# Optimization experiments

Hardware: AMD Instinct MI355X
Metric: run time of the kernel (lower is better)

## Reference

```python
import jax, jax.numpy as jnp
import numpy as np


def _compute_deltas(ts, m):
    """Affine time-decay recurrence: delta_0 = 0; for t>=1:
    delta_t = gap_t + (1 - m_{t-1}) * delta_{t-1}, with gap broadcast over features.
    ts: [b, s] timestamps, m: [b, s, f] float 0/1 mask. Returns [b, s, f]."""
    b, s, f = m.shape
    gaps = ts[:, 1:] - ts[:, :-1]          # [b, s-1]
    a = 1.0 - m[:, :-1, :]                 # [b, s-1, f] decay coefficient

    def step(d, inp):
        g_t, a_t = inp                      # g_t: [b], a_t: [b, f]
        d = g_t[:, None] + a_t * d
        return d, d

    gT = jnp.swapaxes(gaps, 0, 1)          # [s-1, b]
    aT = jnp.swapaxes(a, 0, 1)             # [s-1, b, f]
    _, ds = jax.lax.scan(step, jnp.zeros((b, f), ts.dtype), (gT, aT))
    ds = jnp.swapaxes(ds, 0, 1)            # [b, s-1, f]
    return jnp.concatenate([jnp.zeros((b, 1, f), ts.dtype), ds], axis=1)


def setup_inputs() -> dict:
    key = jax.random.key(0)
    k1, k2, k3 = jax.random.split(key, 3)
    b, s, f = 32, 2048, 768
    # monotonically increasing timestamps (cumsum of positive gaps)
    gaps = jax.random.uniform(k1, (b, s), minval=1.0, maxval=60.0, dtype=jnp.float32)
    timestamps = jnp.cumsum(gaps, axis=1)
    encoded_data = jax.random.normal(k2, (b, s, f), dtype=jnp.float32)
    masks = jax.random.randint(k3, (b, s, f), 0, 2, dtype=jnp.int32)
    return {"timestamps": timestamps, "encoded_data": encoded_data, "masks": masks}


def reference(timestamps, encoded_data, masks):
    """JAX translation of _prepare_brits_data. Returns stacked
    [forward_deltas, backward_deltas, backward_X] of shape [3, b, s, f].
    (forward X / masks are pass-through inputs; backward mask is flip(masks).)"""
    m = masks.astype(timestamps.dtype)
    forward_deltas = _compute_deltas(timestamps, m)
    ts_b = jnp.flip(timestamps, axis=1)
    m_b = jnp.flip(m, axis=1)
    backward_deltas = jnp.abs(_compute_deltas(ts_b, m_b))
    x_b = jnp.flip(encoded_data, axis=1)
    return jnp.stack([forward_deltas, backward_deltas, x_b], axis=0)
```

## Files before the change

### kernel.cpp

```cpp
#include <hip/hip_runtime.h>
#include <stdint.h>

static constexpr int B = 32, S = 2048, F = 768;
static constexpr int CS = 128;
static constexpr int NCH = S / CS;
static constexpr int FT = F / 4;

__device__ __forceinline__ uint32_t getw(const uint4& v, int w) {
    switch (w) { case 0: return v.x; case 1: return v.y; case 2: return v.z; default: return v.w; }
}

__global__ __launch_bounds__(FT) void passA(const int* __restrict__ masks, uint4* __restrict__ bm) {
    const int blk = blockIdx.x;
    const int b = blk / NCH, c = blk % NCH;
    const int j = threadIdx.x;
    const int4* mp = reinterpret_cast<const int4*>(masks + ((size_t)b * S + (size_t)c * CS) * F) + j;
    uint32_t r[4][4];
    #pragma unroll
    for (int w = 0; w < 4; ++w) {
        uint32_t a0 = 0, a1 = 0, a2 = 0, a3 = 0;
        #pragma unroll 8
        for (int k2 = 0; k2 < 32; ++k2) {
            int4 mv = mp[(size_t)(w * 32 + k2) * (F / 4)];
            uint32_t bit = 1u << k2;
            if (mv.x) a0 |= bit;
            if (mv.y) a1 |= bit;
            if (mv.z) a2 |= bit;
            if (mv.w) a3 |= bit;
        }
        r[w][0] = a0; r[w][1] = a1; r[w][2] = a2; r[w][3] = a3;
    }
    uint4* op = bm + (size_t)blk * F + 4 * j;
    #pragma unroll
    for (int q = 0; q < 4; ++q)
        op[q] = make_uint4(r[0][q], r[1][q], r[2][q], r[3][q]);
}

__global__ void passB(const float* __restrict__ ts, const uint4* __restrict__ bm,
                      float* __restrict__ fwdc, float* __restrict__ bwdc) {
    int idx = blockIdx.x * blockDim.x + threadIdx.x;
    if (idx >= B * F) return;
    int b = idx / F, f = idx - b * F;
    const float* tsb = ts + (size_t)b * S;
    float carry = tsb[0];
    for (int c = 0; c < NCH; ++c) {
        fwdc[((size_t)b * NCH + c) * F + f] = carry;
        uint4 v = bm[((size_t)b * NCH + c) * F + f];
        int base = c * CS;
        if (v.w)      carry = tsb[base + 96 + (31 - __clz((int)v.w))];
        else if (v.z) carry = tsb[base + 64 + (31 - __clz((int)v.z))];
        else if (v.y) carry = tsb[base + 32 + (31 - __clz((int)v.y))];
        else if (v.x) carry = tsb[base +      (31 - __clz((int)v.x))];
    }
    carry = tsb[S - 1];
    for (int c = NCH - 1; c >= 0; --c) {
        bwdc[((size_t)b * NCH + c) * F + f] = carry;
        uint4 v = bm[((size_t)b * NCH + c) * F + f];
        int base = c * CS;
        if (v.x)      carry = tsb[base +      (__ffs((int)v.x) - 1)];
        else if (v.y) carry = tsb[base + 32 + (__ffs((int)v.y) - 1)];
        else if (v.z) carry = tsb[base + 64 + (__ffs((int)v.z) - 1)];
        else if (v.w) carry = tsb[base + 96 + (__ffs((int)v.w) - 1)];
    }
}

__global__ __launch_bounds__(FT) void passC(const float* __restrict__ ts, const uint4* __restrict__ bm,
                                            const float* __restrict__ fwdc, const float* __restrict__ bwdc,
                                            float* __restrict__ out0, float* __restrict__ out1) {
    const int blk = blockIdx.x;
    const int b = blk / NCH, c = blk % NCH;
    const int j = threadIdx.x;
    __shared__ float tss[CS];
    for (int k = threadIdx.x; k < CS; k += FT) tss[k] = ts[(size_t)b * S + (size_t)c * CS + k];
    __syncthreads();

    const uint4* bp = bm + (size_t)blk * F + 4 * j;
    uint4 bv0 = bp[0], bv1 = bp[1], bv2 = bp[2], bv3 = bp[3];
    float4 pv = *reinterpret_cast<const float4*>(fwdc + (size_t)blk * F + 4 * j);
    float4 nv = *reinterpret_cast<const float4*>(bwdc + (size_t)blk * F + 4 * j);
    float p0 = pv.x, p1 = pv.y, p2 = pv.z, p3 = pv.w;
    float n0 = nv.x, n1 = nv.y, n2 = nv.z, n3 = nv.w;
    float4* o0 = reinterpret_cast<float4*>(out0 + ((size_t)b * S + (size_t)c * CS) * F) + j;
    float4* o1 = reinterpret_cast<float4*>(out1 + (size_t)b * S * F) + j;

    #pragma unroll
    for (int w = 0; w < 4; ++w) {
        uint32_t b0 = getw(bv0, w), b1 = getw(bv1, w), b2 = getw(bv2, w), b3 = getw(bv3, w);
        #pragma unroll 8
        for (int k2 = 0; k2 < 32; ++k2) {
            int k = w * 32 + k2;
            float t = tss[k];
            o0[(size_t)k * (F / 4)] = make_float4(t - p0, t - p1, t - p2, t - p3);
            p0 = ((b0 >> k2) & 1u) ? t : p0;
            p1 = ((b1 >> k2) & 1u) ? t : p1;
            p2 = ((b2 >> k2) & 1u) ? t : p2;
            p3 = ((b3 >> k2) & 1u) ? t : p3;
        }
    }
    #pragma unroll
    for (int w = 3; w >= 0; --w) {
        uint32_t b0 = getw(bv0, w), b1 = getw(bv1, w), b2 = getw(bv2, w), b3 = getw(bv3, w);
        #pragma unroll 8
        for (int k2 = 31; k2 >= 0; --k2) {
            int k = w * 32 + k2;
            float t = tss[k];
            int rr = (S - 1) - (c * CS + k);
            o1[(size_t)rr * (F / 4)] = make_float4(n0 - t, n1 - t, n2 - t, n3 - t);
            n0 = ((b0 >> k2) & 1u) ? t : n0;
            n1 = ((b1 >> k2) & 1u) ? t : n1;
            n2 = ((b2 >> k2) & 1u) ? t : n2;
            n3 = ((b3 >> k2) & 1u) ? t : n3;
        }
    }
}

__global__ __launch_bounds__(FT) void passD(const float4* __restrict__ x, float4* __restrict__ o2) {
    const int r0 = blockIdx.x * 4;
    const int j = threadIdx.x;
    #pragma unroll
    for (int i = 0; i < 4; ++i) {
        int r = r0 + i;
        int b = r >> 11, t = r & (S - 1);
        int sr = (b << 11) + (S - 1 - t);
        o2[(size_t)r * (F / 4) + j] = x[(size_t)sr * (F / 4) + j];
    }
}

__global__ void fallbackK(const float* __restrict__ ts, const int* __restrict__ masks,
                          float* __restrict__ out0, float* __restrict__ out1) {
    int idx = blockIdx.x * blockDim.x + threadIdx.x;
    if (idx >= B * F) return;
    int b = idx / F, f = idx - b * F;
    const float* tsb = ts + (size_t)b * S;
    const int* mb = masks + (size_t)b * S * F + f;
    float* o0 = out0 + (size_t)b * S * F + f;
    float* o1 = out1 + (size_t)b * S * F + f;
    float prev = tsb[0];
    for (int t = 0; t < S; ++t) {
        float tt = tsb[t];
        o0[(size_t)t * F] = tt - prev;
        if (mb[(size_t)t * F]) prev = tt;
    }
    float nxt = tsb[S - 1];
    for (int t = S - 1; t >= 0; --t) {
        float tt = tsb[t];
        o1[(size_t)(S - 1 - t) * F] = nxt - tt;
        if (mb[(size_t)t * F]) nxt = tt;
    }
}

extern "C" void kernel_launch(void* const* d_in, const int* in_sizes, int n_in,
                              void* d_out, int out_size, void* d_ws, size_t ws_size,
                              hipStream_t stream) {
    const float* ts    = (const float*)d_in[0];
    const float* x     = (const float*)d_in[1];
    const int*   masks = (const int*)d_in[2];
    float* out = (float*)d_out;
    const size_t N = (size_t)B * S * F;

    const size_t bm_bytes    = (size_t)B * NCH * F * sizeof(uint4);
    const size_t carry_elems = (size_t)B * NCH * F;
    const size_t needed      = bm_bytes + 2 * carry_elems * sizeof(float);

    if (ws_size >= needed) {
        uint4* bm   = (uint4*)d_ws;
        float* fwdc = (float*)((char*)d_ws + bm_bytes);
        float* bwdc = fwdc + carry_elems;
        passA<<<B * NCH, FT, 0, stream>>>(masks, bm);
        passB<<<(B * F + 255) / 256, 256, 0, stream>>>(ts, bm, fwdc, bwdc);
        passC<<<B * NCH, FT, 0, stream>>>(ts, bm, fwdc, bwdc, out, out + N);
    } else {
        fallbackK<<<(B * F + 255) / 256, 256, 0, stream>>>(ts, masks, out, out + N);
    }
    passD<<<(B * S) / 4, FT, 0, stream>>>((const float4*)x, (float4*)(out + 2 * N));
}
```

Measured before the change: 239.9 us.

## Fuse mask packing, carry scan, delta output and flip copy into one kernel

Replaces the four-kernel pipeline (bitmask pack, per-chunk carry scan, delta write, reversed copy) with one kernel. Each block handles a 64-step chunk and finds its incoming forward and backward carries by scanning the raw masks outward from the chunk until a set bit is found. The flipped encoded_data copy is done in the same kernel. This removes the workspace bitmask and carry round-trips and several launches, but the carry search costs depend on mask density and can degrade badly for sparse masks.

Result: no change. 238.2 us (-0.7%).

```diff
diff --git a/kernel.cpp b/kernel.cpp
--- a/kernel.cpp
+++ b/kernel.cpp
@@ -2,150 +2,129 @@
 #include <stdint.h>
 
 static constexpr int B = 32, S = 2048, F = 768;
-static constexpr int CS = 128;
-static constexpr int NCH = S / CS;
-static constexpr int FT = F / 4;
+static constexpr int SC = 64;
+static constexpr int NSC = S / SC;
+static constexpr int F4 = F / 4;
+static constexpr int FT = F4;
 
-__device__ __forceinline__ uint32_t getw(const uint4& v, int w) {
-    switch (w) { case 0: return v.x; case 1: return v.y; case 2: return v.z; default: return v.w; }
-}
+__global__ __launch_bounds__(FT) void fusedK(const float* __restrict__ ts,
+                                             const float4* __restrict__ x,
+                                             const int4* __restrict__ masks,
+                                             float* __restrict__ out) {
+    const int blk = blockIdx.x;
+    const int b  = blk >> 5;
+    const int sc = blk & (NSC - 1);
+    const int g0 = sc * SC;
+    const int j  = threadIdx.x;
+    const float* tsb = ts + (size_t)b * S;
+    const int4* mbase = masks + (size_t)b * S * F4 + j;
 
-__global__ __launch_bounds__(FT) void passA(const int* __restrict__ masks, uint4* __restrict__ bm) {
-    const int blk = blockIdx.x;
-    const int b = blk / NCH, c = blk % NCH;
-    const int j = threadIdx.x;
-    const int4* mp = reinterpret_cast<const int4*>(masks + ((size_t)b * S + (size_t)c * CS) * F) + j;
-    uint32_t r[4][4];
-    #pragma unroll
-    for (int w = 0; w < 4; ++w) {
-        uint32_t a0 = 0, a1 = 0, a2 = 0, a3 = 0;
-        #pragma unroll 8
-        for (int k2 = 0; k2 < 32; ++k2) {
-            int4 mv = mp[(size_t)(w * 32 + k2) * (F / 4)];
-            uint32_t bit = 1u << k2;
-            if (mv.x) a0 |= bit;
-            if (mv.y) a1 |= bit;
-            if (mv.z) a2 |= bit;
-            if (mv.w) a3 |= bit;
-        }
-        r[w][0] = a0; r[w][1] = a1; r[w][2] = a2; r[w][3] = a3;
-    }
-    uint4* op = bm + (size_t)blk * F + 4 * j;
-    #pragma unroll
-    for (int q = 0; q < 4; ++q)
-        op[q] = make_uint4(r[0][q], r[1][q], r[2][q], r[3][q]);
-}
-
-__global__ void passB(const float* __restrict__ ts, const uint4* __restrict__ bm,
-                      float* __restrict__ fwdc, float* __restrict__ bwdc) {
-    int idx = blockIdx.x * blockDim.x + threadIdx.x;
-    if (idx >= B * F) return;
-    int b = idx / F, f = idx - b * F;
-    const float* tsb = ts + (size_t)b * S;
-    float carry = tsb[0];
-    for (int c = 0; c < NCH; ++c) {
-        fwdc[((size_t)b * NCH + c) * F + f] = carry;
-        uint4 v = bm[((size_t)b * NCH + c) * F + f];
-        int base = c * CS;
-        if (v.w)      carry = tsb[base + 96 + (31 - __clz((int)v.w))];
-        else if (v.z) carry = tsb[base + 64 + (31 - __clz((int)v.z))];
-        else if (v.y) carry = tsb[base + 32 + (31 - __clz((int)v.y))];
-        else if (v.x) carry = tsb[base +      (31 - __clz((int)v.x))];
-    }
-    carry = tsb[S - 1];
-    for (int c = NCH - 1; c >= 0; --c) {
-        bwdc[((size_t)b * NCH + c) * F + f] = carry;
-        uint4 v = bm[((size_t)b * NCH + c) * F + f];
-        int base = c * CS;
-        if (v.x)      carry = tsb[base +      (__ffs((int)v.x) - 1)];
-        else if (v.y) carry = tsb[base + 32 + (__ffs((int)v.y) - 1)];
-        else if (v.z) carry = tsb[base + 64 + (__ffs((int)v.z) - 1)];
-        else if (v.w) carry = tsb[base + 96 + (__ffs((int)v.w) - 1)];
-    }
-}
-
-__global__ __launch_bounds__(FT) void passC(const float* __restrict__ ts, const uint4* __restrict__ bm,
-                                            const float* __restrict__ fwdc, const float* __restrict__ bwdc,
-                                            float* __restrict__ out0, float* __restrict__ out1) {
-    const int blk = blockIdx.x;
-    const int b = blk / NCH, c = blk % NCH;
-    const int j = threadIdx.x;
-    __shared__ float tss[CS];
-    for (int k = threadIdx.x; k < CS; k += FT) tss[k] = ts[(size_t)b * S + (size_t)c * CS + k];
+    __shared__ float tss[SC];
+    if (threadIdx.x < SC) tss[threadIdx.x] = tsb[g0 + threadIdx.x];
     __syncthreads();
 
-    const uint4* bp = bm + (size_t)blk * F + 4 * j;
-    uint4 bv0 = bp[0], bv1 = bp[1], bv2 = bp[2], bv3 = bp[3];
-    float4 pv = *reinterpret_cast<const float4*>(fwdc + (size_t)blk * F + 4 * j);
-    float4 nv = *reinterpret_cast<const float4*>(bwdc + (size_t)blk * F + 4 * j);
-    float p0 = pv.x, p1 = pv.y, p2 = pv.z, p3 = pv.w;
-    float n0 = nv.x, n1 = nv.y, n2 = nv.z, n3 = nv.w;
-    float4* o0 = reinterpret_cast<float4*>(out0 + ((size_t)b * S + (size_t)c * CS) * F) + j;
-    float4* o1 = reinterpret_cast<float4*>(out1 + (size_t)b * S * F) + j;
+    float t0v = tsb[0];
+    float p0 = t0v, p1 = t0v, p2 = t0v, p3 = t0v;
+    if (g0 > 0) {
+        unsigned um = 0xFu;
+        int r = g0 - 1;
+        while (um && r >= 0) {
+            int rl = (r - 7 > 0) ? r - 7 : 0;
+            int nn = r - rl + 1;
+            int4 mv[8];
+            #pragma unroll
+            for (int q = 0; q < 8; ++q) if (q < nn) mv[q] = mbase[(size_t)(r - q) * F4];
+            #pragma unroll
+            for (int q = 0; q < 8; ++q) if (q < nn) {
+                float t = tsb[r - q];
+                if ((um & 1u) && mv[q].x) { p0 = t; um &= ~1u; }
+                if ((um & 2u) && mv[q].y) { p1 = t; um &= ~2u; }
+                if ((um & 4u) && mv[q].z) { p2 = t; um &= ~4u; }
+                if ((um & 8u) && mv[q].w) { p3 = t; um &= ~8u; }
+            }
+            r = rl - 1;
+        }
+    }
+
+    float tev = tsb[S - 1];
+    float n0 = tev, n1 = tev, n2 = tev, n3 = tev;
+    if (g0 + SC < S) {
+        unsigned um = 0xFu;
+        int r = g0 + SC;
+        while (um && r < S) {
+            int rh = (r + 7 < S - 1) ? r + 7 : S - 1;
+            int nn = rh - r + 1;
+            int4 mv[8];
+            #pragma unroll
+            for (int q = 0; q < 8; ++q) if (q < nn) mv[q] = mbase[(size_t)(r + q) * F4];
+            #pragma unroll
+            for (int q = 0; q < 8; ++q) if (q < nn) {
+                float t = tsb[r + q];
+                if ((um & 1u) && mv[q].x) { n0 = t; um &= ~1u; }
+                if ((um & 2u) && mv[q].y) { n1 = t; um &= ~2u; }
+                if ((um & 4u) && mv[q].z) { n2 = t; um &= ~4u; }
+                if ((um & 8u) && mv[q].w) { n3 = t; um &= ~8u; }
+            }
+            r = rh + 1;
+        }
+    }
+
+    const size_t N4 = (size_t)B * S * F4;
+    float4* o0 = reinterpret_cast<float4*>(out) + (size_t)(b * S + g0) * F4 + j;
+    float4* o1b = reinterpret_cast<float4*>(out) + N4 + (size_t)b * S * F4 + j;
+    float4* o2 = reinterpret_cast<float4*>(out) + 2 * N4 + (size_t)(b * S + g0) * F4 + j;
+    const float4* xb = x + (size_t)b * S * F4 + j;
+
+    uint32_t a0 = 0, a1 = 0, a2 = 0, a3 = 0;
+    #pragma unroll
+    for (int k = 0; k < 32; ++k) {
+        int4 mv = mbase[(size_t)(g0 + k) * F4];
+        float t = tss[k];
+        o0[(size_t)k * F4] = make_float4(t - p0, t - p1, t - p2, t - p3);
+        uint32_t bit = 1u << k;
+        if (mv.x) { a0 |= bit; p0 = t; }
+        if (mv.y) { a1 |= bit; p1 = t; }
+        if (mv.z) { a2 |= bit; p2 = t; }
+        if (mv.w) { a3 |= bit; p3 = t; }
+    }
+    uint32_t c0 = 0, c1 = 0, c2 = 0, c3 = 0;
+    #pragma unroll
+    for (int k = 32; k < 64; ++k) {
+        int4 mv = mbase[(size_t)(g0 + k) * F4];
+        float t = tss[k];
+        o0[(size_t)k * F4] = make_float4(t - p0, t - p1, t - p2, t - p3);
+        uint32_t bit = 1u << (k - 32);
+        if (mv.x) { c0 |= bit; p0 = t; }
+        if (mv.y) { c1 |= bit; p1 = t; }
+        if (mv.z) { c2 |= bit; p2 = t; }
+        if (mv.w) { c3 |= bit; p3 = t; }
+    }
 
     #pragma unroll
-    for (int w = 0; w < 4; ++w) {
-        uint32_t b0 = getw(bv0, w), b1 = getw(bv1, w), b2 = getw(bv2, w), b3 = getw(bv3, w);
-        #pragma unroll 8
-        for (int k2 = 0; k2 < 32; ++k2) {
-            int k = w * 32 + k2;
-            float t = tss[k];
-            o0[(size_t)k * (F / 4)] = make_float4(t - p0, t - p1, t - p2, t - p3);
-            p0 = ((b0 >> k2) & 1u) ? t : p0;
-            p1 = ((b1 >> k2) & 1u) ? t : p1;
-            p2 = ((b2 >> k2) & 1u) ? t : p2;
-            p3 = ((b3 >> k2) & 1u) ? t : p3;
-        }
+    for (int k = 63; k >= 32; --k) {
+        float t = tss[k];
+        size_t fr = (size_t)(S - 1 - g0 - k) * F4;
+        float4 xv = xb[fr];
+        o1b[fr] = make_float4(n0 - t, n1 - t, n2 - t, n3 - t);
+        o2[(size_t)k * F4] = xv;
+        uint32_t bit = 1u << (k - 32);
+        if (c0 & bit) n0 = t;
+        if (c1 & bit) n1 = t;
+        if (c2 & bit) n2 = t;
+        if (c3 & bit) n3 = t;
     }
     #pragma unroll
-    for (int w = 3; w >= 0; --w) {
-        uint32_t b0 = getw(bv0, w), b1 = getw(bv1, w), b2 = getw(bv2, w), b3 = getw(bv3, w);
-        #pragma unroll 8
-        for (int k2 = 31; k2 >= 0; --k2) {
-            int k = w * 32 + k2;
-            float t = tss[k];
-            int rr = (S - 1) - (c * CS + k);
-            o1[(size_t)rr * (F / 4)] = make_float4(n0 - t, n1 - t, n2 - t, n3 - t);
-            n0 = ((b0 >> k2) & 1u) ? t : n0;
-            n1 = ((b1 >> k2) & 1u) ? t : n1;
-            n2 = ((b2 >> k2) & 1u) ? t : n2;
-            n3 = ((b3 >> k2) & 1u) ? t : n3;
-        }
-    }
-}
-
-__global__ __launch_bounds__(FT) void passD(const float4* __restrict__ x, float4* __restrict__ o2) {
-    const int r0 = blockIdx.x * 4;
-    const int j = threadIdx.x;
-    #pragma unroll
-    for (int i = 0; i < 4; ++i) {
-        int r = r0 + i;
-        int b = r >> 11, t = r & (S - 1);
-        int sr = (b << 11) + (S - 1 - t);
-        o2[(size_t)r * (F / 4) + j] = x[(size_t)sr * (F / 4) + j];
-    }
-}
-
-__global__ void fallbackK(const float* __restrict__ ts, const int* __restrict__ masks,
-                          float* __restrict__ out0, float* __restrict__ out1) {
-    int idx = blockIdx.x * blockDim.x + threadIdx.x;
-    if (idx >= B * F) return;
-    int b = idx / F, f = idx - b * F;
-    const float* tsb = ts + (size_t)b * S;
-    const int* mb = masks + (size_t)b * S * F + f;
-    float* o0 = out0 + (size_t)b * S * F + f;
-    float* o1 = out1 + (size_t)b * S * F + f;
-    float prev = tsb[0];
-    for (int t = 0; t < S; ++t) {
-        float tt = tsb[t];
-        o0[(size_t)t * F] = tt - prev;
-        if (mb[(size_t)t * F]) prev = tt;
-    }
-    float nxt = tsb[S - 1];
-    for (int t = S - 1; t >= 0; --t) {
-        float tt = tsb[t];
-        o1[(size_t)(S - 1 - t) * F] = nxt - tt;
-        if (mb[(size_t)t * F]) nxt = tt;
+    for (int k = 31; k >= 0; --k) {
+        float t = tss[k];
+        size_t fr = (size_t)(S - 1 - g0 - k) * F4;
+        float4 xv = xb[fr];
+        o1b[fr] = make_float4(n0 - t, n1 - t, n2 - t, n3 - t);
+        o2[(size_t)k * F4] = xv;
+        uint32_t bit = 1u << k;
+        if (a0 & bit) n0 = t;
+        if (a1 & bit) n1 = t;
+        if (a2 & bit) n2 = t;
+        if (a3 & bit) n3 = t;
     }
 }
 
@@ -153,24 +132,8 @@
                               void* d_out, int out_size, void* d_ws, size_t ws_size,
                               hipStream_t stream) {
     const float* ts    = (const float*)d_in[0];
-    const float* x     = (const float*)d_in[1];
-    const int*   masks = (const int*)d_in[2];
+    const float4* x    = (const float4*)d_in[1];
+    const int4*  masks = (const int4*)d_in[2];
     float* out = (float*)d_out;
-    const size_t N = (size_t)B * S * F;
-
-    const size_t bm_bytes    = (size_t)B * NCH * F * sizeof(uint4);
-    const size_t carry_elems = (size_t)B * NCH * F;
-    const size_t needed      = bm_bytes + 2 * carry_elems * sizeof(float);
-
-    if (ws_size >= needed) {
-        uint4* bm   = (uint4*)d_ws;
-        float* fwdc = (float*)((char*)d_ws + bm_bytes);
-        float* bwdc = fwdc + carry_elems;
-        passA<<<B * NCH, FT, 0, stream>>>(masks, bm);
-        passB<<<(B * F + 255) / 256, 256, 0, stream>>>(ts, bm, fwdc, bwdc);
-        passC<<<B * NCH, FT, 0, stream>>>(ts, bm, fwdc, bwdc, out, out + N);
-    } else {
-        fallbackK<<<(B * F + 255) / 256, 256, 0, stream>>>(ts, masks, out, out + N);
-    }
-    passD<<<(B * S) / 4, FT, 0, stream>>>((const float4*)x, (float4*)(out + 2 * N));
+    fusedK<<<B * NSC, FT, 0, stream>>>(ts, x, masks, out);
 }
```
